# Kernel tuning notes

Measured on AMD Instinct MI355X. Metric: run time of the kernel, lower is better.

The kernel has to match this reference:

```python
import jax, jax.numpy as jnp
import numpy as np

SIGMA = 1e-4
GAMMA = 1e-4
ZNEAR = 1.0
ZFAR = 100.0
EPS = 1e-10

N, H, W, K = 4, 256, 256, 8
V, F, D = 6890, 13776, 16


def setup_inputs() -> dict:
    key = jax.random.key(0)
    k1, k2, k3, k4, k5, k6 = jax.random.split(key, 6)
    vert_features = jax.random.normal(k1, (V, D), dtype=jnp.float32)
    # barycentric coords: positive, sum to 1 over last axis
    b = jax.random.uniform(k2, (N, H, W, K, 3), dtype=jnp.float32, minval=1e-3, maxval=1.0)
    bary_coords = b / jnp.sum(b, axis=-1, keepdims=True)
    # 2D pixel-to-face distances, on the scale of sigma
    dists = jax.random.normal(k3, (N, H, W, K), dtype=jnp.float32) * 1e-4
    # depths within [znear, zfar]
    zbuf = jax.random.uniform(k4, (N, H, W, K), dtype=jnp.float32, minval=ZNEAR, maxval=ZFAR)
    faces = jax.random.randint(k5, (F, 3), 0, V, dtype=jnp.int64)
    # -1 marks pixels not covered by a face (background)
    pix_to_face = jax.random.randint(k6, (N, H, W, K), -1, F, dtype=jnp.int64)
    return {
        "vert_features": vert_features,
        "bary_coords": bary_coords,
        "dists": dists,
        "zbuf": zbuf,
        "faces": faces,
        "pix_to_face": pix_to_face,
    }


def _interpolate_face_attributes(pix_to_face, bary_coords, face_attrs):
    # face_attrs: (F, 3, D); pix_to_face: (N,H,W,K); bary: (N,H,W,K,3)
    idx = jnp.clip(pix_to_face, 0, face_attrs.shape[0] - 1)
    gathered = face_attrs[idx]  # (N,H,W,K,3,D)
    pix = jnp.einsum("nhwkv,nhwkvd->nhwkd", bary_coords, gathered)
    valid = (pix_to_face >= 0).astype(pix.dtype)[..., None]
    return pix * valid  # (N,H,W,K,D)


def _softmax_feature_blend(features, pix_to_face, dists, zbuf, background):
    # features: (N,H,W,K,D)
    dt = features.dtype
    mask = (pix_to_face >= 0).astype(dt)  # (N,H,W,K)
    prob_map = jax.nn.sigmoid(-dists / (SIGMA + 1e-8)) * mask
    alpha = 1.0 - jnp.prod(1.0 - prob_map, axis=-1)  # (N,H,W)
    z_inv = (ZFAR - zbuf) / (ZFAR - ZNEAR) * mask
    z_inv_max = jnp.clip(jnp.max(z_inv, axis=-1, keepdims=True), EPS, None)
    weights_num = prob_map * jnp.exp((z_inv - z_inv_max) / GAMMA)
    delta = jnp.clip(jnp.exp((EPS - z_inv_max) / GAMMA), EPS, None)  # (N,H,W,1)
    denom = jnp.sum(weights_num, axis=-1, keepdims=True) + delta
    weighted = jnp.einsum("nhwk,nhwkd->nhwd", weights_num, features)
    pix = (weighted + delta * background) / denom
    return jnp.concatenate([pix, alpha[..., None]], axis=-1)  # (N,H,W,D+1)


def reference(vert_features, bary_coords, dists, zbuf, faces, pix_to_face):
    face_attrs = vert_features[faces]  # (F,3,D) gather via packed faces
    pix_feats = _interpolate_face_attributes(pix_to_face, bary_coords, face_attrs)
    background = jnp.zeros((vert_features.shape[-1],), dtype=vert_features.dtype)
    out = _softmax_feature_blend(pix_feats, pix_to_face, dists, zbuf, background)
    # (N, D+1, H, W) to mirror the permute((0,3,1,2)) in forward_interpolate
    return jnp.transpose(out, (0, 3, 1, 2))
```

## Files before the change

### kernel.cpp

```cpp
#include <hip/hip_runtime.h>
#include <math.h>

namespace {
constexpr int Nn = 4, Hh = 256, Ww = 256;
constexpr int HW = Hh * Ww;
constexpr int P  = Nn * HW;
constexpr float ZFAR  = 100.0f;
constexpr float ZNEAR = 1.0f;
constexpr float INV_SIG = 1.0f / (1e-4f + 1e-8f);
constexpr float INV_GAM = 1e4f;
constexpr float EPSF    = 1e-10f;
constexpr float INV_ZR  = 1.0f / (ZFAR - ZNEAR);
}

#define QB_I(v, S) __builtin_amdgcn_mov_dpp((v), ((S) * 0x55), 0xf, 0xf, true)
#define QB_F(v, S) __int_as_float(QB_I(__float_as_int(v), S))

#define DO_SLOT(S, PS)                                                         \
    {                                                                          \
        const float ws = QB_F(wb, S);                                          \
        if (ws > 0.0f) {                                                       \
            const int   g0 = QB_I(vx, S);                                      \
            const int   g1 = QB_I(vy, S);                                      \
            const int   g2 = QB_I(vz, S);                                      \
            const float w0 = QB_F(c0, S);                                      \
            const float w1 = QB_F(c1, S);                                      \
            const float w2 = QB_F(c2, S);                                      \
            const float4 r0 = *(reinterpret_cast<const float4*>(vf + (size_t)g0 * 16) + cq); \
            const float4 r1 = *(reinterpret_cast<const float4*>(vf + (size_t)g1 * 16) + cq); \
            const float4 r2 = *(reinterpret_cast<const float4*>(vf + (size_t)g2 * 16) + cq); \
            PS.x = fmaf(w0, r0.x, fmaf(w1, r1.x, fmaf(w2, r2.x, PS.x)));       \
            PS.y = fmaf(w0, r0.y, fmaf(w1, r1.y, fmaf(w2, r2.y, PS.y)));       \
            PS.z = fmaf(w0, r0.z, fmaf(w1, r1.z, fmaf(w2, r2.z, PS.z)));       \
            PS.w = fmaf(w0, r0.w, fmaf(w1, r1.w, fmaf(w2, r2.w, PS.w)));       \
        }                                                                      \
    }

__global__ __launch_bounds__(256) void render_kernel(
    const float* __restrict__ vf,
    const float* __restrict__ bary,
    const float* __restrict__ dists,
    const float* __restrict__ zbuf,
    const int*  __restrict__ faces,
    const int*  __restrict__ p2f,
    float* __restrict__ out)
{
    __shared__ float xp[256 * 20];
    const int pp = threadIdx.x;
    const int p  = blockIdx.x * 256 + pp;
    const int cq = pp & 3;
    const int qb = pp & ~3;

    const int4*   fp = reinterpret_cast<const int4*>(p2f + (size_t)p * 8);
    const float4* zp = reinterpret_cast<const float4*>(zbuf + (size_t)p * 8);
    const float4* dp = reinterpret_cast<const float4*>(dists + (size_t)p * 8);
    int4   fA = fp[0], fB = fp[1];
    float4 zA = zp[0], zB = zp[1];
    float4 dA = dp[0], dB = dp[1];

    int fk[8] = {fA.x, fA.y, fA.z, fA.w, fB.x, fB.y, fB.z, fB.w};
    float zraw[8] = {zA.x, zA.y, zA.z, zA.w, zB.x, zB.y, zB.z, zB.w};
    float dk[8] = {dA.x, dA.y, dA.z, dA.w, dB.x, dB.y, dB.z, dB.w};

    float zi[8];
    float zmax = EPSF;
#pragma unroll
    for (int k = 0; k < 8; ++k) {
        const bool valid = fk[k] >= 0;
        float zv = valid ? (ZFAR - zraw[k]) * INV_ZR : 0.0f;
        zi[k] = zv;
        zmax = fmaxf(zmax, zv);
    }

    const float delta = fmaxf(__expf((EPSF - zmax) * INV_GAM), EPSF);
    float denom = delta;
    float keep  = 1.0f;
    float wv[8];
#pragma unroll
    for (int k = 0; k < 8; ++k) {
        const bool valid = fk[k] >= 0;
        float pr = valid ? 1.0f / (1.0f + __expf(dk[k] * INV_SIG)) : 0.0f;
        keep *= (1.0f - pr);
        float w = pr * __expf((zi[k] - zmax) * INV_GAM);
        wv[k] = w;
        denom += w;
    }

    float4 ps0 = make_float4(0.f, 0.f, 0.f, 0.f);
    float4 ps1 = make_float4(0.f, 0.f, 0.f, 0.f);
    float4 ps2 = make_float4(0.f, 0.f, 0.f, 0.f);
    float4 ps3 = make_float4(0.f, 0.f, 0.f, 0.f);

    while (true) {
        float wb = 0.0f;
        int fsel = 0, ksel = -1;
#pragma unroll
        for (int k = 0; k < 8; ++k) {
            const bool better = wv[k] > wb;
            wb   = better ? wv[k] : wb;
            fsel = better ? fk[k] : fsel;
            ksel = better ? k : ksel;
        }
        if (!__any(wb > 0.0f)) break;

        int vx = 0, vy = 0, vz = 0;
        float c0 = 0.0f, c1 = 0.0f, c2 = 0.0f;
        if (wb > 0.0f) {
            const int4 vidx = *reinterpret_cast<const int4*>(faces + (size_t)fsel * 3);
            const float4 bq = *reinterpret_cast<const float4*>(bary + (size_t)p * 24 + ksel * 3);
            vx = vidx.x; vy = vidx.y; vz = vidx.z;
            c0 = wb * bq.x; c1 = wb * bq.y; c2 = wb * bq.z;
        }

        DO_SLOT(0, ps0)
        DO_SLOT(1, ps1)
        DO_SLOT(2, ps2)
        DO_SLOT(3, ps3)

#pragma unroll
        for (int k = 0; k < 8; ++k)
            wv[k] = (k == ksel) ? 0.0f : wv[k];
    }

    *reinterpret_cast<float4*>(&xp[(qb + 0) * 20 + cq * 4]) = ps0;
    *reinterpret_cast<float4*>(&xp[(qb + 1) * 20 + cq * 4]) = ps1;
    *reinterpret_cast<float4*>(&xp[(qb + 2) * 20 + cq * 4]) = ps2;
    *reinterpret_cast<float4*>(&xp[(qb + 3) * 20 + cq * 4]) = ps3;
    __syncthreads();
    const float4 a0 = *reinterpret_cast<const float4*>(&xp[pp * 20 + 0]);
    const float4 a1 = *reinterpret_cast<const float4*>(&xp[pp * 20 + 4]);
    const float4 a2 = *reinterpret_cast<const float4*>(&xp[pp * 20 + 8]);
    const float4 a3 = *reinterpret_cast<const float4*>(&xp[pp * 20 + 12]);

    const float invden = 1.0f / denom;
    const int n  = p >> 16;
    const int hw = p & (HW - 1);
    float* o = out + (size_t)n * 17 * HW + hw;
    o[(size_t)0  * HW] = a0.x * invden;
    o[(size_t)1  * HW] = a0.y * invden;
    o[(size_t)2  * HW] = a0.z * invden;
    o[(size_t)3  * HW] = a0.w * invden;
    o[(size_t)4  * HW] = a1.x * invden;
    o[(size_t)5  * HW] = a1.y * invden;
    o[(size_t)6  * HW] = a1.z * invden;
    o[(size_t)7  * HW] = a1.w * invden;
    o[(size_t)8  * HW] = a2.x * invden;
    o[(size_t)9  * HW] = a2.y * invden;
    o[(size_t)10 * HW] = a2.z * invden;
    o[(size_t)11 * HW] = a2.w * invden;
    o[(size_t)12 * HW] = a3.x * invden;
    o[(size_t)13 * HW] = a3.y * invden;
    o[(size_t)14 * HW] = a3.z * invden;
    o[(size_t)15 * HW] = a3.w * invden;
    o[(size_t)16 * HW] = 1.0f - keep;
}

extern "C" void kernel_launch(void* const* d_in, const int* in_sizes, int n_in,
                              void* d_out, int out_size, void* d_ws, size_t ws_size,
                              hipStream_t stream) {
    const float* vf    = (const float*)d_in[0];
    const float* bary  = (const float*)d_in[1];
    const float* dists = (const float*)d_in[2];
    const float* zbuf  = (const float*)d_in[3];
    const int*   faces = (const int*)d_in[4];
    const int*   p2f   = (const int*)d_in[5];
    float* out = (float*)d_out;

    render_kernel<<<dim3(P / 256), dim3(256), 0, stream>>>(
        vf, bary, dists, zbuf, faces, p2f, out);
}
```

Measured before the change: 21.17 us.

## Prefetch top-depth face features before weight computation to overlap gather latency

Chooses the face with the highest inverse depth while computing zmax, then issues its face-index, barycentric and vertex-feature gathers before the sigmoid and exp weight computation, so memory latency overlaps with ALU work. The first FMA pass uses these prefetched loads, and the old iterative selection loop is kept only as a fallback for any remaining nonzero weights. This relies on the top-z face usually holding the dominant weight, since GAMMA makes the others underflow. It adds register pressure from twelve prefetched float4 values, which may lower occupancy.

```diff
diff --git a/kernel.cpp b/kernel.cpp
--- a/kernel.cpp
+++ b/kernel.cpp
@@ -16,16 +16,40 @@
 #define QB_I(v, S) __builtin_amdgcn_mov_dpp((v), ((S) * 0x55), 0xf, 0xf, true)
 #define QB_F(v, S) __int_as_float(QB_I(__float_as_int(v), S))
 
+#define LOAD_SLOT(S, QA, QB_, QC, OK)                                          \
+    {                                                                          \
+        OK = QB_I(fvalid, S);                                                  \
+        if (OK) {                                                              \
+            const int g0 = QB_I(vx, S);                                        \
+            const int g1 = QB_I(vy, S);                                        \
+            const int g2 = QB_I(vz, S);                                        \
+            QA = *(reinterpret_cast<const float4*>(vf + (size_t)g0 * 16) + cq); \
+            QB_ = *(reinterpret_cast<const float4*>(vf + (size_t)g1 * 16) + cq); \
+            QC = *(reinterpret_cast<const float4*>(vf + (size_t)g2 * 16) + cq); \
+        }                                                                      \
+    }
+
+#define FMA_SLOT(S, QA, QB_, QC, PS)                                           \
+    {                                                                          \
+        const float w0 = QB_F(c0, S);                                          \
+        const float w1 = QB_F(c1, S);                                          \
+        const float w2 = QB_F(c2, S);                                          \
+        PS.x = fmaf(w0, QA.x, fmaf(w1, QB_.x, fmaf(w2, QC.x, PS.x)));          \
+        PS.y = fmaf(w0, QA.y, fmaf(w1, QB_.y, fmaf(w2, QC.y, PS.y)));          \
+        PS.z = fmaf(w0, QA.z, fmaf(w1, QB_.z, fmaf(w2, QC.z, PS.z)));          \
+        PS.w = fmaf(w0, QA.w, fmaf(w1, QB_.w, fmaf(w2, QC.w, PS.w)));          \
+    }
+
 #define DO_SLOT(S, PS)                                                         \
     {                                                                          \
-        const float ws = QB_F(wb, S);                                          \
+        const float ws = QB_F(wb2, S);                                         \
         if (ws > 0.0f) {                                                       \
-            const int   g0 = QB_I(vx, S);                                      \
-            const int   g1 = QB_I(vy, S);                                      \
-            const int   g2 = QB_I(vz, S);                                      \
-            const float w0 = QB_F(c0, S);                                      \
-            const float w1 = QB_F(c1, S);                                      \
-            const float w2 = QB_F(c2, S);                                      \
+            const int   g0 = QB_I(vx2, S);                                     \
+            const int   g1 = QB_I(vy2, S);                                     \
+            const int   g2 = QB_I(vz2, S);                                     \
+            const float w0 = QB_F(e0, S);                                      \
+            const float w1 = QB_F(e1, S);                                      \
+            const float w2 = QB_F(e2, S);                                      \
             const float4 r0 = *(reinterpret_cast<const float4*>(vf + (size_t)g0 * 16) + cq); \
             const float4 r1 = *(reinterpret_cast<const float4*>(vf + (size_t)g1 * 16) + cq); \
             const float4 r2 = *(reinterpret_cast<const float4*>(vf + (size_t)g2 * 16) + cq); \
@@ -60,18 +84,45 @@
 
     int fk[8] = {fA.x, fA.y, fA.z, fA.w, fB.x, fB.y, fB.z, fB.w};
     float zraw[8] = {zA.x, zA.y, zA.z, zA.w, zB.x, zB.y, zB.z, zB.w};
-    float dk[8] = {dA.x, dA.y, dA.z, dA.w, dB.x, dB.y, dB.z, dB.w};
 
     float zi[8];
-    float zmax = EPSF;
+    float zmax = EPSF, zbest = 0.0f;
+    int ksel = -1, fsel = 0;
 #pragma unroll
     for (int k = 0; k < 8; ++k) {
         const bool valid = fk[k] >= 0;
         float zv = valid ? (ZFAR - zraw[k]) * INV_ZR : 0.0f;
         zi[k] = zv;
         zmax = fmaxf(zmax, zv);
-    }
-
+        const bool better = valid && (zv > zbest);
+        zbest = better ? zv : zbest;
+        ksel  = better ? k : ksel;
+        fsel  = better ? fk[k] : fsel;
+    }
+    const int fvalid = (ksel >= 0) ? 1 : 0;
+
+    int vx = 0, vy = 0, vz = 0;
+    float b0 = 0.0f, b1 = 0.0f, b2 = 0.0f;
+    if (fvalid) {
+        const int4 vidx = *reinterpret_cast<const int4*>(faces + (size_t)fsel * 3);
+        const float4 bq = *reinterpret_cast<const float4*>(bary + (size_t)p * 24 + ksel * 3);
+        vx = vidx.x; vy = vidx.y; vz = vidx.z;
+        b0 = bq.x; b1 = bq.y; b2 = bq.z;
+    }
+
+    float4 z4 = make_float4(0.f, 0.f, 0.f, 0.f);
+    float4 q0a = z4, q0b = z4, q0c = z4;
+    float4 q1a = z4, q1b = z4, q1c = z4;
+    float4 q2a = z4, q2b = z4, q2c = z4;
+    float4 q3a = z4, q3b = z4, q3c = z4;
+    int ok0, ok1, ok2, ok3;
+    LOAD_SLOT(0, q0a, q0b, q0c, ok0)
+    LOAD_SLOT(1, q1a, q1b, q1c, ok1)
+    LOAD_SLOT(2, q2a, q2b, q2c, ok2)
+    LOAD_SLOT(3, q3a, q3b, q3c, ok3)
+    (void)ok0; (void)ok1; (void)ok2; (void)ok3;
+
+    float dk[8] = {dA.x, dA.y, dA.z, dA.w, dB.x, dB.y, dB.z, dB.w};
     const float delta = fmaxf(__expf((EPSF - zmax) * INV_GAM), EPSF);
     float denom = delta;
     float keep  = 1.0f;
@@ -86,40 +137,53 @@
         denom += w;
     }
 
-    float4 ps0 = make_float4(0.f, 0.f, 0.f, 0.f);
-    float4 ps1 = make_float4(0.f, 0.f, 0.f, 0.f);
-    float4 ps2 = make_float4(0.f, 0.f, 0.f, 0.f);
-    float4 ps3 = make_float4(0.f, 0.f, 0.f, 0.f);
-
-    while (true) {
-        float wb = 0.0f;
-        int fsel = 0, ksel = -1;
-#pragma unroll
-        for (int k = 0; k < 8; ++k) {
-            const bool better = wv[k] > wb;
-            wb   = better ? wv[k] : wb;
-            fsel = better ? fk[k] : fsel;
-            ksel = better ? k : ksel;
+    float wb = 0.0f;
+#pragma unroll
+    for (int k = 0; k < 8; ++k) wb = (k == ksel) ? wv[k] : wb;
+    const float c0 = wb * b0, c1 = wb * b1, c2 = wb * b2;
+
+    float4 ps0 = z4, ps1 = z4, ps2 = z4, ps3 = z4;
+    FMA_SLOT(0, q0a, q0b, q0c, ps0)
+    FMA_SLOT(1, q1a, q1b, q1c, ps1)
+    FMA_SLOT(2, q2a, q2b, q2c, ps2)
+    FMA_SLOT(3, q3a, q3b, q3c, ps3)
+
+#pragma unroll
+    for (int k = 0; k < 8; ++k) wv[k] = (k == ksel) ? 0.0f : wv[k];
+    bool more = false;
+#pragma unroll
+    for (int k = 0; k < 8; ++k) more = more || (wv[k] > 0.0f);
+
+    if (__any(more)) {
+        while (true) {
+            float wb2 = 0.0f;
+            int fsel2 = 0, ksel2 = -1;
+#pragma unroll
+            for (int k = 0; k < 8; ++k) {
+                const bool better = wv[k] > wb2;
+                wb2   = better ? wv[k] : wb2;
+                fsel2 = better ? fk[k] : fsel2;
+                ksel2 = better ? k : ksel2;
+            }
+            if (!__any(wb2 > 0.0f)) break;
+
+            int vx2 = 0, vy2 = 0, vz2 = 0;
+            float e0 = 0.0f, e1 = 0.0f, e2 = 0.0f;
+            if (wb2 > 0.0f) {
+                const int4 vidx = *reinterpret_cast<const int4*>(faces + (size_t)fsel2 * 3);
+                const float4 bq = *reinterpret_cast<const float4*>(
+                    bary + (size_t)p * 24 + ksel2 * 3);
+                vx2 = vidx.x; vy2 = vidx.y; vz2 = vidx.z;
+                e0 = wb2 * bq.x; e1 = wb2 * bq.y; e2 = wb2 * bq.z;
+            }
+            DO_SLOT(0, ps0)
+            DO_SLOT(1, ps1)
+            DO_SLOT(2, ps2)
+            DO_SLOT(3, ps3)
+#pragma unroll
+            for (int k = 0; k < 8; ++k)
+                wv[k] = (k == ksel2) ? 0.0f : wv[k];
         }
-        if (!__any(wb > 0.0f)) break;
-
-        int vx = 0, vy = 0, vz = 0;
-        float c0 = 0.0f, c1 = 0.0f, c2 = 0.0f;
-        if (wb > 0.0f) {
-            const int4 vidx = *reinterpret_cast<const int4*>(faces + (size_t)fsel * 3);
-            const float4 bq = *reinterpret_cast<const float4*>(bary + (size_t)p * 24 + ksel * 3);
-            vx = vidx.x; vy = vidx.y; vz = vidx.z;
-            c0 = wb * bq.x; c1 = wb * bq.y; c2 = wb * bq.z;
-        }
-
-        DO_SLOT(0, ps0)
-        DO_SLOT(1, ps1)
-        DO_SLOT(2, ps2)
-        DO_SLOT(3, ps3)
-
-#pragma unroll
-        for (int k = 0; k < 8; ++k)
-            wv[k] = (k == ksel) ? 0.0f : wv[k];
     }
 
     *reinterpret_cast<float4*>(&xp[(qb + 0) * 20 + cq * 4]) = ps0;
```

New measurement: 20.76 us. 1.02x faster.
